# Performance work log

Measured on AMD Instinct MI355X. Metric: run time of the kernel, lower is better.

## Reference

```python
import jax, jax.numpy as jnp
import numpy as np

EMBED_DIM = 1024
NUM_HEADS = 16
HEAD_DIM = EMBED_DIM // NUM_HEADS
SCALING = HEAD_DIM ** -0.5
EPS = 1e-5


def _rope(seq_len):
    inv_freq = 1.0 / (10000.0 ** (jnp.arange(0, HEAD_DIM, 2, dtype=jnp.float32) / HEAD_DIM))
    freqs = jnp.arange(seq_len, dtype=jnp.float32)[:, None] * inv_freq[None, :]
    emb = jnp.concatenate([freqs, freqs], axis=-1)  # (S, HEAD_DIM)
    return jnp.cos(emb), jnp.sin(emb)


def _rotate(x, cos, sin):
    # x: (B,H,S,Dh), cos/sin: (S,Dh)
    d = x.shape[-1]
    x1, x2 = x[..., : d // 2], x[..., d // 2 :]
    rotated = jnp.concatenate([-x2, x1], axis=-1)
    return x * cos + rotated * sin


def setup_inputs() -> dict:
    key = jax.random.key(0)
    ks = jax.random.split(key, 6)
    B, S, D = 2, 2048, EMBED_DIM
    scale = D ** -0.5
    return {
        "x": jax.random.normal(ks[0], (B, S, D), jnp.float32),
        "Wq": jax.random.normal(ks[1], (D, D), jnp.float32) * scale,
        "Wk": jax.random.normal(ks[2], (D, D), jnp.float32) * scale,
        "Wv": jax.random.normal(ks[3], (D, D), jnp.float32) * scale,
        "Wg": jax.random.normal(ks[4], (D, D), jnp.float32) * scale,
        "Wo": jax.random.normal(ks[5], (D, D), jnp.float32) * scale,
        "gn_w": jnp.ones((D,), jnp.float32),
        "gn_b": jnp.zeros((D,), jnp.float32),
    }


def reference(x, Wq, Wk, Wv, Wg, Wo, gn_w, gn_b):
    B, S, D = x.shape
    H, Dh = NUM_HEADS, HEAD_DIM

    def split_heads(t):  # (B,S,D) -> (B,H,S,Dh)
        return t.reshape(B, S, H, Dh).transpose(0, 2, 1, 3)

    q = split_heads(x @ Wq.T)
    k = split_heads(x @ Wk.T)
    v = split_heads(x @ Wv.T)

    cos, sin = _rope(S)
    q = _rotate(q, cos, sin)
    k = _rotate(k, cos, sin)

    retention = jnp.einsum("bhsd,bhtd->bhst", q, k) * SCALING

    # multiplicative causal decay mask: gamma**(n-m) for n>=m else 0
    gammas = (1.0 - 2.0 ** (-5.0 - jnp.arange(H, dtype=jnp.float32)))  # (H,)
    diff = jnp.arange(S)[:, None] - jnp.arange(S)[None, :]             # (S,S)
    causal = diff >= 0
    decay = jnp.where(causal, gammas[:, None, None] ** jnp.maximum(diff, 0).astype(jnp.float32), 0.0)  # (H,S,S)
    retention = retention * decay[None]

    out = jnp.einsum("bhst,bhtd->bhsd", retention, v)  # (B,H,S,Dh)
    out = out.transpose(0, 2, 1, 3).reshape(B * S, H, Dh)

    # GroupNorm with num_groups == H over channel dim D
    mean = out.mean(axis=-1, keepdims=True)
    var = out.var(axis=-1, keepdims=True)
    out = (out - mean) * jax.lax.rsqrt(var + EPS)
    out = out * gn_w.reshape(H, Dh) + gn_b.reshape(H, Dh)
    out = out.reshape(B, S, D)

    gate = jax.nn.silu(x @ Wg.T)
    return (gate * out) @ Wo.T
```

## Files before the change

kernel.cpp:

```cpp
#include <hip/hip_runtime.h>
#include <cstdint>
#include <cstddef>


typedef __attribute__((ext_vector_type(4))) float  f32x4;
typedef __attribute__((ext_vector_type(8))) short  bf16x8;
typedef __attribute__((ext_vector_type(4))) short  bf16x4v;
typedef __attribute__((ext_vector_type(2))) unsigned int u32x2;

#define MFMA_BF16 __builtin_amdgcn_mfma_f32_16x16x32_bf16

__device__ __forceinline__ unsigned short f2bf(float f) {
    unsigned u = __float_as_uint(f);
    u += 0x7fffu + ((u >> 16) & 1u);
    return (unsigned short)(u >> 16);
}
__device__ __forceinline__ float bf2f(unsigned short h) {
    return __uint_as_float(((unsigned)h) << 16);
}
__device__ __forceinline__ unsigned cvt_pk_bf16(float lo, float hi) {
    unsigned r;
    asm("v_cvt_pk_bf16_f32 %0, %1, %2" : "=v"(r) : "v"(lo), "v"(hi));
    return r;
}

__global__ void convert_kernel(const float* __restrict__ x,
                               const float* __restrict__ wq, const float* __restrict__ wk,
                               const float* __restrict__ wv, const float* __restrict__ wg,
                               const float* __restrict__ wo,
                               unsigned short* __restrict__ dst) {
    const size_t total = 4194304u + 5u * 1048576u;
    for (size_t i = (size_t)blockIdx.x * blockDim.x + threadIdx.x;
         i * 4 < total; i += (size_t)gridDim.x * blockDim.x) {
        size_t e = i * 4;
        const float* src; size_t off;
        if (e < 4194304u) { src = x; off = e; }
        else {
            size_t r = e - 4194304u;
            int w = (int)(r >> 20); off = r & 1048575u;
            src = (w == 0) ? wq : (w == 1) ? wk : (w == 2) ? wv : (w == 3) ? wg : wo;
        }
        f32x4 v = *(const f32x4*)(src + off);
        unsigned short o0 = f2bf(v[0]), o1 = f2bf(v[1]), o2 = f2bf(v[2]), o3 = f2bf(v[3]);
        unsigned long long pack = (unsigned long long)o0 | ((unsigned long long)o1 << 16)
                                | ((unsigned long long)o2 << 32) | ((unsigned long long)o3 << 48);
        *(unsigned long long*)(dst + e) = pack;
    }
}

__global__ void rope_tables(float* __restrict__ cosT, float* __restrict__ sinT) {
    int i = blockIdx.x * blockDim.x + threadIdx.x;
    if (i >= 2048 * 32) return;
    int s = i >> 5, j = i & 31;
    float inv = exp2f(-(float)j * (13.287712379549449f / 32.0f));
    float ang = (float)s * inv;
    cosT[i] = cosf(ang);
    sinT[i] = sinf(ang);
}

__launch_bounds__(256, 2)
__global__ void gemm_fused(const unsigned short* __restrict__ A_x,
                           const unsigned short* __restrict__ A_a2,
                           const unsigned short* __restrict__ Wq, const unsigned short* __restrict__ Wk,
                           const unsigned short* __restrict__ Wv, const unsigned short* __restrict__ Wg,
                           const unsigned short* __restrict__ Wo,
                           const float* __restrict__ cosT, const float* __restrict__ sinT,
                           unsigned short* __restrict__ q_hm, unsigned short* __restrict__ k_hm,
                           unsigned short* __restrict__ kTs, unsigned short* __restrict__ vT,
                           unsigned short* __restrict__ gate,
                           float* __restrict__ outf,
                           int mode_base) {
    int mode = mode_base + blockIdx.z;
    const unsigned short* A = (mode == 4) ? A_a2 : A_x;
    const unsigned short* W = (mode == 0) ? Wq : (mode == 1) ? Wk :
                              (mode == 2) ? Wv : (mode == 3) ? Wg : Wo;

    __shared__ __align__(16) unsigned short Ash[128 * 64];
    __shared__ __align__(16) unsigned short Bsh[128 * 64];

    int tid = threadIdx.x;
    int lane = tid & 63, wid = tid >> 6;
    int wm = wid >> 1, wn = wid & 1;
    int m0 = blockIdx.y * 128, n0 = blockIdx.x * 128;

    f32x4 acc[4][4];
#pragma unroll
    for (int i = 0; i < 4; ++i)
#pragma unroll
        for (int j = 0; j < 4; ++j)
#pragma unroll
            for (int r = 0; r < 4; ++r) acc[i][j][r] = 0.0f;

    for (int k0 = 0; k0 < 1024; k0 += 64) {
        __syncthreads();
#pragma unroll
        for (int t = 0; t < 4; ++t) {
            int chunk = tid + t * 256;
            int row = chunk >> 3, c = chunk & 7;
            bf16x8 va = *(const bf16x8*)(A + (size_t)(m0 + row) * 1024 + k0 + c * 8);
            *(bf16x8*)&Ash[row * 64 + ((c ^ (row & 7)) << 3)] = va;
            bf16x8 vb = *(const bf16x8*)(W + (size_t)(n0 + row) * 1024 + k0 + c * 8);
            *(bf16x8*)&Bsh[row * 64 + ((c ^ (row & 7)) << 3)] = vb;
        }
        __syncthreads();
#pragma unroll
        for (int ks = 0; ks < 2; ++ks) {
            bf16x8 af[4], bfv[4];
#pragma unroll
            for (int mi = 0; mi < 4; ++mi) {
                int row = wm * 64 + mi * 16 + (lane & 15);
                int c = ks * 4 + (lane >> 4);
                af[mi] = *(const bf16x8*)&Ash[row * 64 + ((c ^ (row & 7)) << 3)];
            }
#pragma unroll
            for (int ni = 0; ni < 4; ++ni) {
                int row = wn * 64 + ni * 16 + (lane & 15);
                int c = ks * 4 + (lane >> 4);
                bfv[ni] = *(const bf16x8*)&Bsh[row * 64 + ((c ^ (row & 7)) << 3)];
            }
            if (mode == 2) {
#pragma unroll
                for (int mi = 0; mi < 4; ++mi)
#pragma unroll
                    for (int ni = 0; ni < 4; ++ni)
                        acc[mi][ni] = MFMA_BF16(bfv[ni], af[mi], acc[mi][ni], 0, 0, 0);
            } else {
#pragma unroll
                for (int mi = 0; mi < 4; ++mi)
#pragma unroll
                    for (int ni = 0; ni < 4; ++ni)
                        acc[mi][ni] = MFMA_BF16(af[mi], bfv[ni], acc[mi][ni], 0, 0, 0);
            }
        }
    }

    int mbase = m0 + wm * 64, nbase = n0 + wn * 64;
    int g4 = (lane >> 4) << 2;

    if (mode == 0 || mode == 1) {
        unsigned short* dst = (mode == 0) ? q_hm : k_hm;
#pragma unroll
        for (int mi = 0; mi < 4; ++mi)
#pragma unroll
            for (int ni = 0; ni < 4; ++ni)
#pragma unroll
                for (int r = 0; r < 4; ++r) {
                    int m = mbase + mi * 16 + g4 + r;
                    int n = nbase + ni * 16 + (lane & 15);
                    int s = m & 2047, b = m >> 11, h = n >> 6, d = n & 63, j = d & 31;
                    float v  = acc[mi][ni][r];
                    float v2 = acc[mi][ni ^ 2][r];
                    float cs = cosT[s * 32 + j], sn = sinT[s * 32 + j];
                    float rot = (d < 32) ? -v2 : v2;
                    float o = v * cs + rot * sn;
                    dst[((size_t)(b * 16 + h) * 2048 + s) * 64 + d] = f2bf(o);
                    if (mode == 1) {
                        float lg = log2f(1.0f - exp2f(-5.0f - (float)h));
                        float scl = exp2f(lg * (float)(63 - (s & 63)));
                        kTs[((size_t)((b * 16 + h) * 64 + d)) * 2048 + s] = f2bf(o * scl);
                    }
                }
    } else if (mode == 2) {
#pragma unroll
        for (int mi = 0; mi < 4; ++mi)
#pragma unroll
            for (int ni = 0; ni < 4; ++ni)
#pragma unroll
                for (int r = 0; r < 4; ++r) {
                    int n = nbase + ni * 16 + g4 + r;
                    int m = mbase + mi * 16 + (lane & 15);
                    int b = m >> 11, s = m & 2047, h = n >> 6, d = n & 63;
                    vT[((size_t)((b * 16 + h) * 64 + d)) * 2048 + s] = f2bf(acc[mi][ni][r]);
                }
    } else if (mode == 3) {
#pragma unroll
        for (int mi = 0; mi < 4; ++mi)
#pragma unroll
            for (int ni = 0; ni < 4; ++ni)
#pragma unroll
                for (int r = 0; r < 4; ++r) {
                    int m = mbase + mi * 16 + g4 + r;
                    int n = nbase + ni * 16 + (lane & 15);
                    float v = acc[mi][ni][r];
                    gate[(size_t)m * 1024 + n] = f2bf(v / (1.0f + expf(-v)));
                }
    } else {
#pragma unroll
        for (int mi = 0; mi < 4; ++mi)
#pragma unroll
            for (int ni = 0; ni < 4; ++ni)
#pragma unroll
                for (int r = 0; r < 4; ++r) {
                    int m = mbase + mi * 16 + g4 + r;
                    int n = nbase + ni * 16 + (lane & 15);
                    outf[(size_t)m * 1024 + n] = acc[mi][ni][r];
                }
    }
}

__launch_bounds__(256, 4)
__global__ void chunk_state_kernel(const unsigned short* __restrict__ vT,
                                   const unsigned short* __restrict__ kTs,
                                   unsigned short* __restrict__ LT) {
    int tid = threadIdx.x, lane = tid & 63, wid = tid >> 6;
    int bh = blockIdx.x >> 3;
    int c  = (blockIdx.x & 7) * 4 + wid;
    int q_lane = lane & 15;
    int g4 = (lane >> 4) << 2, g8 = (lane >> 4) << 3;

    const unsigned short* vb = vT  + (size_t)bh * 131072 + (size_t)c * 64;
    const unsigned short* kb = kTs + (size_t)bh * 131072 + (size_t)c * 64;

    f32x4 acc[4][4];
#pragma unroll
    for (int i = 0; i < 4; ++i)
#pragma unroll
        for (int j = 0; j < 4; ++j)
#pragma unroll
            for (int r = 0; r < 4; ++r) acc[i][j][r] = 0.0f;

#pragma unroll
    for (int ks = 0; ks < 2; ++ks) {
        bf16x8 a[4], bv[4];
#pragma unroll
        for (int mi = 0; mi < 4; ++mi)
            a[mi] = *(const bf16x8*)(vb + (size_t)(mi * 16 + q_lane) * 2048 + ks * 32 + g8);
#pragma unroll
        for (int ni = 0; ni < 4; ++ni)
            bv[ni] = *(const bf16x8*)(kb + (size_t)(ni * 16 + q_lane) * 2048 + ks * 32 + g8);
#pragma unroll
        for (int mi = 0; mi < 4; ++mi)
#pragma unroll
            for (int ni = 0; ni < 4; ++ni)
                acc[mi][ni] = MFMA_BF16(a[mi], bv[ni], acc[mi][ni], 0, 0, 0);
    }

    unsigned short* lp = LT + ((size_t)(bh * 32 + c)) * 4096;
#pragma unroll
    for (int mi = 0; mi < 4; ++mi)
#pragma unroll
        for (int ni = 0; ni < 4; ++ni)
#pragma unroll
            for (int r = 0; r < 4; ++r) {
                int d2 = mi * 16 + g4 + r;
                int d1 = ni * 16 + q_lane;
                lp[d2 * 64 + d1] = f2bf(acc[mi][ni][r]);
            }
}

__launch_bounds__(256, 4)
__global__ void scan_kernel(const unsigned short* __restrict__ LT,
                            unsigned short* __restrict__ ST) {
    int bh = blockIdx.x >> 2;
    int e0 = ((blockIdx.x & 3) * 256 + threadIdx.x) * 4;
    int h = bh & 15;
    float lg2g = log2f(1.0f - exp2f(-5.0f - (float)h));
    float g64 = exp2f(64.0f * lg2g);

    float s0 = 0.f, s1 = 0.f, s2 = 0.f, s3 = 0.f;
    const unsigned short* lp = LT + (size_t)bh * 32 * 4096 + e0;
    unsigned short* sp = ST + (size_t)bh * 32 * 4096 + e0;
    for (int c = 0; c < 32; ++c) {
        u32x2 wv;
        wv[0] = cvt_pk_bf16(s0, s1);
        wv[1] = cvt_pk_bf16(s2, s3);
        *(u32x2*)sp = wv;
        bf16x4v lv = *(const bf16x4v*)lp;
        s0 = s0 * g64 + bf2f((unsigned short)lv[0]);
        s1 = s1 * g64 + bf2f((unsigned short)lv[1]);
        s2 = s2 * g64 + bf2f((unsigned short)lv[2]);
        s3 = s3 * g64 + bf2f((unsigned short)lv[3]);
        lp += 4096; sp += 4096;
    }
}

__launch_bounds__(256, 4)
__global__ void retention_chunk_kernel(const unsigned short* __restrict__ qh,
                                       const unsigned short* __restrict__ kh,
                                       const unsigned short* __restrict__ vT,
                                       const unsigned short* __restrict__ ST,
                                       const float* __restrict__ gn_w, const float* __restrict__ gn_b,
                                       const unsigned short* __restrict__ gate,
                                       unsigned short* __restrict__ a2) {
    __shared__ __align__(16) unsigned short Ssh[4][16 * 40];

    int tid = threadIdx.x, lane = tid & 63, wid = tid >> 6;
    int c = blockIdx.x, bh = blockIdx.y;
    int b = bh >> 4, h = bh & 15;

    float lg2g = log2f(1.0f - exp2f(-5.0f - (float)h));
    float gam1 = exp2f(lg2g);
    float gmr1 = exp2f(-lg2g);
    float gmr2 = gmr1 * gmr1, gmr3 = gmr2 * gmr1;
    float gmr16 = exp2f(-16.0f * lg2g);

    int q_lane = lane & 15;
    int g4 = (lane >> 4) << 2, g8 = (lane >> 4) << 3;
    int i_col = wid * 16 + q_lane;
    int s_abs = c * 64 + i_col;

    bf16x8 aq0, aq1;
    {
        const unsigned short* qp = qh + ((size_t)bh * 2048 + s_abs) * 64 + g8;
        aq0 = *(const bf16x8*)(qp);
        aq1 = *(const bf16x8*)(qp + 32);
    }

    f32x4 z4 = {0.f, 0.f, 0.f, 0.f};
    f32x4 o0, o1, o2, o3;

    {
        const unsigned short* stp = ST + ((size_t)(bh * 32 + c)) * 4096
                                  + (size_t)q_lane * 64 + g8;
        bf16x8 s00 = *(const bf16x8*)(stp);
        bf16x8 s01 = *(const bf16x8*)(stp + 32);
        bf16x8 s10 = *(const bf16x8*)(stp + 1024);
        bf16x8 s11 = *(const bf16x8*)(stp + 1056);
        bf16x8 s20 = *(const bf16x8*)(stp + 2048);
        bf16x8 s21 = *(const bf16x8*)(stp + 2080);
        bf16x8 s30 = *(const bf16x8*)(stp + 3072);
        bf16x8 s31 = *(const bf16x8*)(stp + 3104);
        o0 = MFMA_BF16(aq0, s00, z4, 0, 0, 0); o0 = MFMA_BF16(aq1, s01, o0, 0, 0, 0);
        o1 = MFMA_BF16(aq0, s10, z4, 0, 0, 0); o1 = MFMA_BF16(aq1, s11, o1, 0, 0, 0);
        o2 = MFMA_BF16(aq0, s20, z4, 0, 0, 0); o2 = MFMA_BF16(aq1, s21, o2, 0, 0, 0);
        o3 = MFMA_BF16(aq0, s30, z4, 0, 0, 0); o3 = MFMA_BF16(aq1, s31, o3, 0, 0, 0);
    }
    {
        float cs0 = 0.125f * exp2f(lg2g * (float)(wid * 16 + g4 + 1));
        float cs1 = cs0 * gam1, cs2 = cs1 * gam1, cs3 = cs2 * gam1;
        o0[0] *= cs0; o0[1] *= cs1; o0[2] *= cs2; o0[3] *= cs3;
        o1[0] *= cs0; o1[1] *= cs1; o1[2] *= cs2; o1[3] *= cs3;
        o2[0] *= cs0; o2[1] *= cs1; o2[2] *= cs2; o2[3] *= cs3;
        o3[0] *= cs0; o3[1] *= cs1; o3[2] *= cs2; o3[3] *= cs3;
    }

    const unsigned short* kbase = kh + ((size_t)bh * 2048 + c * 64) * 64;
    const unsigned short* vbase = vT + (size_t)bh * 131072 + c * 64;
    unsigned short* ssw = &Ssh[wid][0];
    int ntt = (wid >> 1) + 1;
    for (int tt = 0; tt < ntt; ++tt) {
        int tbase = tt * 32;
        const unsigned short* kp = kbase + (size_t)(tbase + q_lane) * 64 + g8;
        bf16x8 k00 = *(const bf16x8*)(kp);
        bf16x8 k01 = *(const bf16x8*)(kp + 32);
        bf16x8 k10 = *(const bf16x8*)(kp + 1024);
        bf16x8 k11 = *(const bf16x8*)(kp + 1056);
        f32x4 sc0 = z4, sc1 = z4;
        sc0 = MFMA_BF16(k00, aq0, sc0, 0, 0, 0);
        sc0 = MFMA_BF16(k01, aq1, sc0, 0, 0, 0);
        sc1 = MFMA_BF16(k10, aq0, sc1, 0, 0, 0);
        sc1 = MFMA_BF16(k11, aq1, sc1, 0, 0, 0);

        int j0 = tbase + g4;
        float e0 = 0.125f * exp2f(lg2g * (float)(i_col - j0));
        float e1 = e0 * gmr1, e2 = e0 * gmr2, e3 = e0 * gmr3;
        float v00 = (i_col >= j0    ) ? sc0[0] * e0 : 0.0f;
        float v01 = (i_col >= j0 + 1) ? sc0[1] * e1 : 0.0f;
        float v02 = (i_col >= j0 + 2) ? sc0[2] * e2 : 0.0f;
        float v03 = (i_col >= j0 + 3) ? sc0[3] * e3 : 0.0f;
        int j1 = j0 + 16;
        float f0 = e0 * gmr16, f1 = e1 * gmr16, f2 = e2 * gmr16, f3 = e3 * gmr16;
        float v10 = (i_col >= j1    ) ? sc1[0] * f0 : 0.0f;
        float v11 = (i_col >= j1 + 1) ? sc1[1] * f1 : 0.0f;
        float v12 = (i_col >= j1 + 2) ? sc1[2] * f2 : 0.0f;
        float v13 = (i_col >= j1 + 3) ? sc1[3] * f3 : 0.0f;

        u32x2 wA, wB;
        wA[0] = cvt_pk_bf16(v00, v01); wA[1] = cvt_pk_bf16(v02, v03);
        wB[0] = cvt_pk_bf16(v10, v11); wB[1] = cvt_pk_bf16(v12, v13);
        *(u32x2*)&ssw[q_lane * 40 + g4] = wA;
        *(u32x2*)&ssw[q_lane * 40 + 16 + g4] = wB;

        bf16x8 sf = *(const bf16x8*)&ssw[q_lane * 40 + g8];
        bf16x8 bv0 = *(const bf16x8*)(vbase + (size_t)(q_lane) * 2048 + tbase + g8);
        bf16x8 bv1 = *(const bf16x8*)(vbase + (size_t)(16 + q_lane) * 2048 + tbase + g8);
        bf16x8 bv2 = *(const bf16x8*)(vbase + (size_t)(32 + q_lane) * 2048 + tbase + g8);
        bf16x8 bv3 = *(const bf16x8*)(vbase + (size_t)(48 + q_lane) * 2048 + tbase + g8);
        o0 = MFMA_BF16(sf, bv0, o0, 0, 0, 0);
        o1 = MFMA_BF16(sf, bv1, o1, 0, 0, 0);
        o2 = MFMA_BF16(sf, bv2, o2, 0, 0, 0);
        o3 = MFMA_BF16(sf, bv3, o3, 0, 0, 0);
    }

    float mean[4], rstd[4];
#pragma unroll
    for (int r = 0; r < 4; ++r) {
        float s1 = o0[r] + o1[r] + o2[r] + o3[r];
        float s2 = o0[r]*o0[r] + o1[r]*o1[r] + o2[r]*o2[r] + o3[r]*o3[r];
#pragma unroll
        for (int m = 1; m < 16; m <<= 1) {
            s1 += __shfl_xor(s1, m);
            s2 += __shfl_xor(s2, m);
        }
        float mu = s1 * 0.015625f;
        mean[r] = mu;
        float var = s2 * 0.015625f - mu * mu;
        rstd[r] = rsqrtf(var + 1e-5f);
    }
    int srow = c * 64 + wid * 16;
#define RT_STORE(OV, DB)                                                    \
    {                                                                       \
        int d = DB * 16 + q_lane;                                           \
        float gw = gn_w[h * 64 + d];                                        \
        float gb = gn_b[h * 64 + d];                                        \
        _Pragma("unroll")                                                   \
        for (int r = 0; r < 4; ++r) {                                       \
            int s_out = srow + g4 + r;                                      \
            size_t gi = ((size_t)(b * 2048 + s_out)) * 1024 + h * 64 + d;   \
            float val = (OV[r] - mean[r]) * rstd[r] * gw + gb;              \
            val *= bf2f(gate[gi]);                                          \
            a2[gi] = f2bf(val);                                             \
        }                                                                   \
    }
    RT_STORE(o0, 0); RT_STORE(o1, 1); RT_STORE(o2, 2); RT_STORE(o3, 3);
#undef RT_STORE
}

extern "C" void kernel_launch(void* const* d_in, const int* in_sizes, int n_in,
                              void* d_out, int out_size, void* d_ws, size_t ws_size,
                              hipStream_t stream) {
    const float* x    = (const float*)d_in[0];
    const float* Wq   = (const float*)d_in[1];
    const float* Wk   = (const float*)d_in[2];
    const float* Wv   = (const float*)d_in[3];
    const float* Wg   = (const float*)d_in[4];
    const float* Wo   = (const float*)d_in[5];
    const float* gn_w = (const float*)d_in[6];
    const float* gn_b = (const float*)d_in[7];

    unsigned short* xb   = (unsigned short*)d_ws;
    unsigned short* wqb  = xb  + 4194304;
    unsigned short* wkb  = wqb + 1048576;
    unsigned short* wvb  = wkb + 1048576;
    unsigned short* wgb  = wvb + 1048576;
    unsigned short* wob  = wgb + 1048576;
    float*          cosT = (float*)(wob + 1048576);
    float*          sinT = cosT + 65536;
    unsigned short* q_hm = (unsigned short*)(sinT + 65536);
    unsigned short* k_hm = q_hm + 4194304;
    unsigned short* vTb  = k_hm + 4194304;
    unsigned short* kTs  = vTb + 4194304;
    unsigned short* a2   = kTs + 4194304;
    unsigned short* gate = a2  + 4194304;
    unsigned short* LT   = a2;
    unsigned short* ST   = xb;

    float* outf = (float*)d_out;

    convert_kernel<<<dim3(2048), dim3(256), 0, stream>>>(x, Wq, Wk, Wv, Wg, Wo, xb);
    rope_tables<<<dim3(256), dim3(256), 0, stream>>>(cosT, sinT);
    gemm_fused<<<dim3(8, 32, 4), dim3(256), 0, stream>>>(
        xb, a2, wqb, wkb, wvb, wgb, wob, cosT, sinT,
        q_hm, k_hm, kTs, vTb, gate, outf, 0);
    chunk_state_kernel<<<dim3(256), dim3(256), 0, stream>>>(vTb, kTs, LT);
    scan_kernel<<<dim3(128), dim3(256), 0, stream>>>(LT, ST);
    retention_chunk_kernel<<<dim3(32, 32), dim3(256), 0, stream>>>(
        q_hm, k_hm, vTb, ST, gn_w, gn_b, gate, a2);
    gemm_fused<<<dim3(8, 32, 1), dim3(256), 0, stream>>>(
        xb, a2, wqb, wkb, wvb, wgb, wob, cosT, sinT,
        q_hm, k_hm, kTs, vTb, gate, outf, 4);
}
```

Before: 125.7 us.

## Load GEMM tiles via direct global-to-LDS loads and precompute decay scales

Replaces the register-staged global-to-shared tile copies in the projection GEMM with global_load_lds 16-byte direct loads. The XOR swizzle moves to the source address so the LDS layout stays the same. It also hoists the per-element log2/exp2 decay scale for the scaled K transpose into a few per-thread precomputed factors that are reused through multiplication. This saves VGPR staging and instructions but relies on the lane-to-LDS mapping matching the swizzle, and the repeated multiplications may differ slightly in rounding.

```diff
diff --git a/kernel.cpp b/kernel.cpp
--- a/kernel.cpp
+++ b/kernel.cpp
@@ -9,6 +9,10 @@
 typedef __attribute__((ext_vector_type(2))) unsigned int u32x2;
 
 #define MFMA_BF16 __builtin_amdgcn_mfma_f32_16x16x32_bf16
+
+#define GLL16(gp, lp) __builtin_amdgcn_global_load_lds( \
+    (const __attribute__((address_space(1))) unsigned int*)(const void*)(gp), \
+    (__attribute__((address_space(3))) unsigned int*)(void*)(lp), 16, 0, 0)
 
 __device__ __forceinline__ unsigned short f2bf(float f) {
     unsigned u = __float_as_uint(f);
@@ -83,6 +87,11 @@
     int wm = wid >> 1, wn = wid & 1;
     int m0 = blockIdx.y * 128, n0 = blockIdx.x * 128;
 
+    int l_row = lane >> 3;
+    int l_src = ((lane & 7) ^ l_row) << 3;
+    const unsigned short* Ab = A + (size_t)(m0 + wid * 32 + l_row) * 1024 + l_src;
+    const unsigned short* Wb = W + (size_t)(n0 + wid * 32 + l_row) * 1024 + l_src;
+
     f32x4 acc[4][4];
 #pragma unroll
     for (int i = 0; i < 4; ++i)
@@ -94,13 +103,9 @@
     for (int k0 = 0; k0 < 1024; k0 += 64) {
         __syncthreads();
 #pragma unroll
-        for (int t = 0; t < 4; ++t) {
-            int chunk = tid + t * 256;
-            int row = chunk >> 3, c = chunk & 7;
-            bf16x8 va = *(const bf16x8*)(A + (size_t)(m0 + row) * 1024 + k0 + c * 8);
-            *(bf16x8*)&Ash[row * 64 + ((c ^ (row & 7)) << 3)] = va;
-            bf16x8 vb = *(const bf16x8*)(W + (size_t)(n0 + row) * 1024 + k0 + c * 8);
-            *(bf16x8*)&Bsh[row * 64 + ((c ^ (row & 7)) << 3)] = vb;
+        for (int i = 0; i < 4; ++i) {
+            GLL16(Ab + (size_t)(i * 8) * 1024 + k0, &Ash[(wid * 32 + i * 8) * 64]);
+            GLL16(Wb + (size_t)(i * 8) * 1024 + k0, &Bsh[(wid * 32 + i * 8) * 64]);
         }
         __syncthreads();
 #pragma unroll
@@ -139,6 +144,14 @@
 
     if (mode == 0 || mode == 1) {
         unsigned short* dst = (mode == 0) ? q_hm : k_hm;
+        float sr[4] = {1.f, 1.f, 1.f, 1.f}, m16p[4] = {1.f, 1.f, 1.f, 1.f};
+        if (mode == 1) {
+            float lg = log2f(1.0f - exp2f(-5.0f - (float)(nbase >> 6)));
+            float gm1 = exp2f(-lg), gm16 = exp2f(-16.0f * lg);
+            sr[0] = exp2f(lg * (float)(63 - g4));
+            sr[1] = sr[0] * gm1; sr[2] = sr[1] * gm1; sr[3] = sr[2] * gm1;
+            m16p[1] = gm16; m16p[2] = gm16 * gm16; m16p[3] = m16p[2] * gm16;
+        }
 #pragma unroll
         for (int mi = 0; mi < 4; ++mi)
 #pragma unroll
@@ -155,9 +168,8 @@
                     float o = v * cs + rot * sn;
                     dst[((size_t)(b * 16 + h) * 2048 + s) * 64 + d] = f2bf(o);
                     if (mode == 1) {
-                        float lg = log2f(1.0f - exp2f(-5.0f - (float)h));
-                        float scl = exp2f(lg * (float)(63 - (s & 63)));
-                        kTs[((size_t)((b * 16 + h) * 64 + d)) * 2048 + s] = f2bf(o * scl);
+                        kTs[((size_t)((b * 16 + h) * 64 + d)) * 2048 + s]
+                            = f2bf(o * (sr[r] * m16p[mi]));
                     }
                 }
     } else if (mode == 2) {
```

Measured after the change: 120.3 us. -4.3%, faster.
